# Kernel optimization log

Hardware: AMD Instinct MI355X
Metric: run time of the kernel (lower is better)

The kernel has to match this reference:

```python
import jax, jax.numpy as jnp
import numpy as np

NODE_FEATURES = 256
HIDDEN = 32
N_NODES = 100000
N_EDGES = 3200000


def _glorot(key, shape):
    fan_in, fan_out = shape[-2], shape[-1]
    lim = (6.0 / (fan_in + fan_out)) ** 0.5
    return jax.random.uniform(key, shape, jnp.float32, -lim, lim)


def setup_inputs() -> dict:
    key = jax.random.key(0)
    ks = jax.random.split(key, 12)
    in_cat = NODE_FEATURES + HIDDEN  # DConv input is cat([X, H])
    x = jax.random.normal(ks[0], (N_NODES, NODE_FEATURES), jnp.float32)
    edge_index = jax.random.randint(ks[1], (2, N_EDGES), 0, N_NODES, jnp.int64)
    return {
        "x": x,
        "edge_index": edge_index,
        # DConv weights have shape (2, K=1, in, out); squeeze K -> (2, in, out)
        "w_z": _glorot(ks[2], (2, in_cat, HIDDEN)),
        "b_z": jnp.zeros((HIDDEN,), jnp.float32),
        "w_r": _glorot(ks[3], (2, in_cat, HIDDEN)),
        "b_r": jnp.zeros((HIDDEN,), jnp.float32),
        "w_h": _glorot(ks[4], (2, in_cat, HIDDEN)),
        "b_h": jnp.zeros((HIDDEN,), jnp.float32),
        # fc head, stored as [in, out]
        "fc1_w": _glorot(ks[5], (HIDDEN, HIDDEN)),
        "fc1_b": jnp.zeros((HIDDEN,), jnp.float32),
        "fc2_w": _glorot(ks[6], (HIDDEN, 1)),
        "fc2_b": jnp.zeros((1,), jnp.float32),
    }


def _dconv_k1(inp, w, b):
    # K=1 DConv: only the k=0 Chebyshev term for both diffusion directions,
    # i.e. no propagation over edges. H = X @ W_out + X @ W_in + bias.
    return inp @ (w[0] + w[1]) + b


def reference(x, edge_index, w_z, b_z, w_r, b_r, w_h, b_h, fc1_w, fc1_b, fc2_w, fc2_b):
    n = x.shape[0]
    h0 = jnp.zeros((n, HIDDEN), x.dtype)  # DCRNN called with H=None -> zeros
    xh0 = jnp.concatenate([x, h0], axis=1)  # [N, F+H]
    z = jax.nn.sigmoid(_dconv_k1(xh0, w_z, b_z))  # update gate
    r = jax.nn.sigmoid(_dconv_k1(xh0, w_r, b_r))  # reset gate
    xrh = jnp.concatenate([x, r * h0], axis=1)
    h_tilde = jnp.tanh(_dconv_k1(xrh, w_h, b_h))
    h = z * h0 + (1.0 - z) * h_tilde  # [N, 32]
    # fc head: Linear-ReLU-Dropout(eval=identity)-Linear-Sigmoid
    hidden = jax.nn.relu(h @ fc1_w + fc1_b)
    out = jax.nn.sigmoid(hidden @ fc2_w + fc2_b)  # [N, 1]
    return out
```

## Files before the change

### kernel.cpp

```cpp
#include <hip/hip_runtime.h>
#include <hip/hip_bf16.h>


#define NF   256
#define NOUT 64
#define TN   128
#define BK   64
#define ROWPAD (BK + 1)
#define NTHR 256

__global__ void prep_W(const float* __restrict__ wz,
                       const float* __restrict__ wh,
                       float* __restrict__ W)
{
    int idx = blockIdx.x * blockDim.x + threadIdx.x;
    if (idx >= NF * NOUT) return;
    int k = idx >> 6;
    int o = idx & 63;
    const int PLANE = 288 * 32;
    float v;
    if (o < 32) v = wz[k * 32 + o]        + wz[PLANE + k * 32 + o];
    else        v = wh[k * 32 + (o - 32)] + wh[PLANE + k * 32 + (o - 32)];
    W[idx] = v;
}

__device__ __forceinline__ float fast_sigmoid(float v) {
    return 1.0f / (1.0f + __expf(-v));
}
__device__ __forceinline__ float fast_tanh(float v) {
    return 1.0f - 2.0f / (1.0f + __expf(2.0f * v));
}

__global__ void __launch_bounds__(NTHR, 2)
rgcn_main(const float* __restrict__ x,
          const float* __restrict__ W,
          const float* __restrict__ bz,
          const float* __restrict__ bh,
          const float* __restrict__ fc1w,
          const float* __restrict__ fc1b,
          const float* __restrict__ fc2w,
          const float* __restrict__ fc2b,
          float* __restrict__ out,
          int n_nodes)
{
    __shared__ float Xs[TN * ROWPAD];

    const int tid   = threadIdx.x;
    const int nl    = tid & (TN - 1);
    const int half  = __builtin_amdgcn_readfirstlane(tid >> 7);
    const int node0 = blockIdx.x * TN;
    const int node  = node0 + nl;

    float acc[32];
#pragma unroll
    for (int i = 0; i < 32; ++i) acc[i] = 0.0f;

    const float* Wh = W + half * 32;

    for (int k0 = 0; k0 < NF; k0 += BK) {
        __syncthreads();
#pragma unroll
        for (int i = 0; i < 8; ++i) {
            int q  = tid + i * NTHR;
            int nn = q >> 4;
            int kk = q & 15;
            float4 v = make_float4(0.f, 0.f, 0.f, 0.f);
            int gn = node0 + nn;
            if (gn < n_nodes)
                v = *(const float4*)(x + (size_t)gn * NF + k0 + kk * 4);
            float* dst = &Xs[nn * ROWPAD + kk * 4];
            dst[0] = v.x; dst[1] = v.y; dst[2] = v.z; dst[3] = v.w;
        }
        __syncthreads();

        for (int k = 0; k < BK; ++k) {
            float a = Xs[nl * ROWPAD + k];
            const float4* wr = (const float4*)(Wh + (size_t)(k0 + k) * NOUT);
#pragma unroll
            for (int o4 = 0; o4 < 8; ++o4) {
                float4 w = wr[o4];
                acc[o4 * 4 + 0] = fmaf(a, w.x, acc[o4 * 4 + 0]);
                acc[o4 * 4 + 1] = fmaf(a, w.y, acc[o4 * 4 + 1]);
                acc[o4 * 4 + 2] = fmaf(a, w.z, acc[o4 * 4 + 2]);
                acc[o4 * 4 + 3] = fmaf(a, w.w, acc[o4 * 4 + 3]);
            }
        }
    }

    __syncthreads();
    float* Hs = Xs;

    if (half == 1 && node < n_nodes) {
#pragma unroll
        for (int o = 0; o < 32; ++o)
            Hs[nl * 33 + o] = fast_tanh(acc[o] + bh[o]);
    }
    __syncthreads();

    if (half == 0 && node < n_nodes) {
        float h[32];
#pragma unroll
        for (int o = 0; o < 32; ++o) {
            float z = fast_sigmoid(acc[o] + bz[o]);
            h[o] = (1.0f - z) * Hs[nl * 33 + o];
        }
        float oacc = fc2b[0];
        for (int j = 0; j < 32; ++j) {
            float s = fc1b[j];
#pragma unroll
            for (int o = 0; o < 32; ++o)
                s = fmaf(h[o], fc1w[o * 32 + j], s);
            s = fmaxf(s, 0.0f);
            oacc = fmaf(s, fc2w[j], oacc);
        }
        out[node] = fast_sigmoid(oacc);
    }
}

extern "C" void kernel_launch(void* const* d_in, const int* in_sizes, int n_in,
                              void* d_out, int out_size, void* d_ws, size_t ws_size,
                              hipStream_t stream) {
    const float* x    = (const float*)d_in[0];
    const float* wz   = (const float*)d_in[2];
    const float* bz   = (const float*)d_in[3];
    const float* wh   = (const float*)d_in[6];
    const float* bh   = (const float*)d_in[7];
    const float* fc1w = (const float*)d_in[8];
    const float* fc1b = (const float*)d_in[9];
    const float* fc2w = (const float*)d_in[10];
    const float* fc2b = (const float*)d_in[11];
    float* out = (float*)d_out;
    float* W   = (float*)d_ws;

    const int n = in_sizes[0] / NF;

    prep_W<<<(NF * NOUT + 255) / 256, 256, 0, stream>>>(wz, wh, W);
    rgcn_main<<<(n + TN - 1) / TN, NTHR, 0, stream>>>(
        x, W, bz, bh, fc1w, fc1b, fc2w, fc2b, out, n);
}
```

Before: 247.0 us.

## Use 2D register-tiled GEMM with shared-memory W and interleaved gate columns

The GEMM is restructured from one node per thread with W read straight from global memory into a 2D register tile: each thread computes 8 nodes by 4 outputs, with transposed X tiles and W tiles staged in shared memory. prep_W permutes the weight columns so each thread holds the matching z and h columns for its two hidden units, which lets the gating run without a cross-half shared-memory exchange. The FC head is split across both thread halves and the partial sums are combined in shared memory. Smaller shared memory and launch bounds of 4 aim to raise occupancy and cut redundant global W loads, at the cost of more syncs and a more complex index mapping.

```diff
diff --git a/kernel.cpp b/kernel.cpp
--- a/kernel.cpp
+++ b/kernel.cpp
@@ -2,26 +2,31 @@
 #include <hip/hip_bf16.h>
 
 
-#define NF   256
-#define NOUT 64
-#define TN   128
-#define BK   64
-#define ROWPAD (BK + 1)
-#define NTHR 256
+#define NF    256
+#define NOUT  64
+#define MB    128
+#define BK    32
+#define NTHR  256
+#define XPAD  132
+#define WPAD  68
+#define HPAD  34
+#define S_FLOATS 6400
 
 __global__ void prep_W(const float* __restrict__ wz,
                        const float* __restrict__ wh,
-                       float* __restrict__ W)
+                       float* __restrict__ Wp)
 {
     int idx = blockIdx.x * blockDim.x + threadIdx.x;
     if (idx >= NF * NOUT) return;
     int k = idx >> 6;
-    int o = idx & 63;
+    int j = idx & 63;
+    int tx = j >> 2, m = j & 3;
+    int o = 2 * tx + (m & 1) + ((m >> 1) << 5);
     const int PLANE = 288 * 32;
     float v;
     if (o < 32) v = wz[k * 32 + o]        + wz[PLANE + k * 32 + o];
     else        v = wh[k * 32 + (o - 32)] + wh[PLANE + k * 32 + (o - 32)];
-    W[idx] = v;
+    Wp[idx] = v;
 }
 
 __device__ __forceinline__ float fast_sigmoid(float v) {
@@ -31,9 +36,9 @@
     return 1.0f - 2.0f / (1.0f + __expf(2.0f * v));
 }
 
-__global__ void __launch_bounds__(NTHR, 2)
+__global__ void __launch_bounds__(NTHR, 4)
 rgcn_main(const float* __restrict__ x,
-          const float* __restrict__ W,
+          const float* __restrict__ Wp,
           const float* __restrict__ bz,
           const float* __restrict__ bh,
           const float* __restrict__ fc1w,
@@ -43,77 +48,104 @@
           float* __restrict__ out,
           int n_nodes)
 {
-    __shared__ float Xs[TN * ROWPAD];
+    __shared__ float S[S_FLOATS];
+    float* XsT = S;
+    float* Ws  = S + BK * XPAD;
 
     const int tid   = threadIdx.x;
-    const int nl    = tid & (TN - 1);
-    const int half  = __builtin_amdgcn_readfirstlane(tid >> 7);
-    const int node0 = blockIdx.x * TN;
-    const int node  = node0 + nl;
+    const int tx    = tid & 15;
+    const int ty    = tid >> 4;
+    const int node0 = blockIdx.x * MB;
 
     float acc[32];
 #pragma unroll
     for (int i = 0; i < 32; ++i) acc[i] = 0.0f;
 
-    const float* Wh = W + half * 32;
-
     for (int k0 = 0; k0 < NF; k0 += BK) {
         __syncthreads();
 #pragma unroll
-        for (int i = 0; i < 8; ++i) {
-            int q  = tid + i * NTHR;
-            int nn = q >> 4;
-            int kk = q & 15;
+        for (int i = 0; i < 4; ++i) {
+            int q    = tid + i * NTHR;
+            int nn   = q >> 3;
+            int slot = q & 7;
             float4 v = make_float4(0.f, 0.f, 0.f, 0.f);
             int gn = node0 + nn;
             if (gn < n_nodes)
-                v = *(const float4*)(x + (size_t)gn * NF + k0 + kk * 4);
-            float* dst = &Xs[nn * ROWPAD + kk * 4];
-            dst[0] = v.x; dst[1] = v.y; dst[2] = v.z; dst[3] = v.w;
+                v = *(const float4*)(x + (size_t)gn * NF + k0 + slot * 4);
+            XsT[(slot * 4 + 0) * XPAD + nn] = v.x;
+            XsT[(slot * 4 + 1) * XPAD + nn] = v.y;
+            XsT[(slot * 4 + 2) * XPAD + nn] = v.z;
+            XsT[(slot * 4 + 3) * XPAD + nn] = v.w;
+        }
+#pragma unroll
+        for (int i = 0; i < 2; ++i) {
+            int q  = tid + i * NTHR;
+            int r  = q >> 4;
+            int cs = q & 15;
+            float4 v = *(const float4*)(Wp + (size_t)(k0 + r) * NOUT + cs * 4);
+            *(float4*)(Ws + r * WPAD + cs * 4) = v;
         }
         __syncthreads();
 
+#pragma unroll
         for (int k = 0; k < BK; ++k) {
-            float a = Xs[nl * ROWPAD + k];
-            const float4* wr = (const float4*)(Wh + (size_t)(k0 + k) * NOUT);
+            const float* xr = XsT + k * XPAD + ty * 8;
+            float4 a0 = *(const float4*)(xr);
+            float4 a1 = *(const float4*)(xr + 4);
+            float4 w  = *(const float4*)(Ws + k * WPAD + tx * 4);
+            float a[8] = {a0.x, a0.y, a0.z, a0.w, a1.x, a1.y, a1.z, a1.w};
 #pragma unroll
-            for (int o4 = 0; o4 < 8; ++o4) {
-                float4 w = wr[o4];
-                acc[o4 * 4 + 0] = fmaf(a, w.x, acc[o4 * 4 + 0]);
-                acc[o4 * 4 + 1] = fmaf(a, w.y, acc[o4 * 4 + 1]);
-                acc[o4 * 4 + 2] = fmaf(a, w.z, acc[o4 * 4 + 2]);
-                acc[o4 * 4 + 3] = fmaf(a, w.w, acc[o4 * 4 + 3]);
+            for (int i = 0; i < 8; ++i) {
+                acc[i * 4 + 0] = fmaf(a[i], w.x, acc[i * 4 + 0]);
+                acc[i * 4 + 1] = fmaf(a[i], w.y, acc[i * 4 + 1]);
+                acc[i * 4 + 2] = fmaf(a[i], w.z, acc[i * 4 + 2]);
+                acc[i * 4 + 3] = fmaf(a[i], w.w, acc[i * 4 + 3]);
             }
         }
     }
 
     __syncthreads();
-    float* Hs = Xs;
+    float* Hs = S;
+    float* Ps = S + MB * HPAD;
 
-    if (half == 1 && node < n_nodes) {
+    const float bz0 = bz[2 * tx], bz1 = bz[2 * tx + 1];
+    const float bh0 = bh[2 * tx], bh1 = bh[2 * tx + 1];
 #pragma unroll
-        for (int o = 0; o < 32; ++o)
-            Hs[nl * 33 + o] = fast_tanh(acc[o] + bh[o]);
+    for (int i = 0; i < 8; ++i) {
+        int nl = ty * 8 + i;
+        float z0 = fast_sigmoid(acc[i * 4 + 0] + bz0);
+        float z1 = fast_sigmoid(acc[i * 4 + 1] + bz1);
+        float t0 = fast_tanh   (acc[i * 4 + 2] + bh0);
+        float t1 = fast_tanh   (acc[i * 4 + 3] + bh1);
+        Hs[nl * HPAD + 2 * tx]     = (1.0f - z0) * t0;
+        Hs[nl * HPAD + 2 * tx + 1] = (1.0f - z1) * t1;
     }
     __syncthreads();
 
-    if (half == 0 && node < n_nodes) {
-        float h[32];
+    const int nl   = tid & (MB - 1);
+    const int half = tid >> 7;
+    float h[32];
 #pragma unroll
-        for (int o = 0; o < 32; ++o) {
-            float z = fast_sigmoid(acc[o] + bz[o]);
-            h[o] = (1.0f - z) * Hs[nl * 33 + o];
-        }
-        float oacc = fc2b[0];
-        for (int j = 0; j < 32; ++j) {
-            float s = fc1b[j];
+    for (int m = 0; m < 8; ++m) {
+        float4 v = *(const float4*)(Hs + nl * HPAD + m * 4);
+        h[m * 4 + 0] = v.x; h[m * 4 + 1] = v.y;
+        h[m * 4 + 2] = v.z; h[m * 4 + 3] = v.w;
+    }
+    float part = 0.0f;
+    for (int jj = 0; jj < 16; ++jj) {
+        int j = half * 16 + jj;
+        float s = fc1b[j];
 #pragma unroll
-            for (int o = 0; o < 32; ++o)
-                s = fmaf(h[o], fc1w[o * 32 + j], s);
-            s = fmaxf(s, 0.0f);
-            oacc = fmaf(s, fc2w[j], oacc);
-        }
-        out[node] = fast_sigmoid(oacc);
+        for (int o = 0; o < 32; ++o)
+            s = fmaf(h[o], fc1w[o * 32 + j], s);
+        part = fmaf(fmaxf(s, 0.0f), fc2w[j], part);
+    }
+    if (half == 1) Ps[nl] = part;
+    __syncthreads();
+    if (half == 0) {
+        int gn = node0 + nl;
+        if (gn < n_nodes)
+            out[gn] = fast_sigmoid(part + Ps[nl] + fc2b[0]);
     }
 }
 
@@ -130,11 +162,11 @@
     const float* fc2w = (const float*)d_in[10];
     const float* fc2b = (const float*)d_in[11];
     float* out = (float*)d_out;
-    float* W   = (float*)d_ws;
+    float* Wp  = (float*)d_ws;
 
     const int n = in_sizes[0] / NF;
 
-    prep_W<<<(NF * NOUT + 255) / 256, 256, 0, stream>>>(wz, wh, W);
-    rgcn_main<<<(n + TN - 1) / TN, NTHR, 0, stream>>>(
-        x, W, bz, bh, fc1w, fc1b, fc2w, fc2b, out, n);
+    prep_W<<<(NF * NOUT + 255) / 256, 256, 0, stream>>>(wz, wh, Wp);
+    rgcn_main<<<(n + MB - 1) / MB, NTHR, 0, stream>>>(
+        x, Wp, bz, bh, fc1w, fc1b, fc2w, fc2b, out, n);
 }
```

Result: faster. 220.1 us (-10.9%).
